# Performance work log

Hardware: AMD Instinct MI355X
Metric: run time of the kernel (lower is better)

Reference implementation:

```python
import jax, jax.numpy as jnp
import numpy as np

NCODEBOOKS, K, SUBVEC = 32, 16, 128
IN_F, OUT_F = 4096, 2048
BATCH, SEQ = 2, 1024


def setup_inputs() -> dict:
    key = jax.random.key(0)
    k1, k2, k3, k4, k5 = jax.random.split(key, 5)
    return {
        "x": jax.random.normal(k1, (BATCH, SEQ, IN_F), dtype=jnp.float32),
        "centroids": jax.random.normal(k2, (NCODEBOOKS, K, SUBVEC), dtype=jnp.float32),
        "weight": jax.random.normal(k3, (NCODEBOOKS, SUBVEC, OUT_F), dtype=jnp.float32),
        "inverse_temperature_logit": jax.random.normal(k4, (1,), dtype=jnp.float32),
        "bias": jax.random.normal(k5, (OUT_F,), dtype=jnp.float32),
    }


def reference(x, centroids, weight, inverse_temperature_logit, bias):
    shape = x.shape[:-1]
    C, k, d = centroids.shape
    # [N, C, d] -> [C, N, d]
    xr = jnp.transpose(x.reshape(-1, C, d), (1, 0, 2))
    # Euclidean cdist per codebook: [C, N, k]
    x2 = jnp.sum(xr * xr, axis=-1)[:, :, None]
    c2 = jnp.sum(centroids * centroids, axis=-1)[:, None, :]
    xc = jnp.einsum('cnd,ckd->cnk', xr, centroids)
    dist = jnp.sqrt(jnp.maximum(x2 + c2 - 2.0 * xc, 0.0))
    inv_temp = jax.nn.softplus(inverse_temperature_logit) + 1.0  # [1]
    attention = jax.nn.softmax(-dist * inv_temp, axis=-1)  # [C, N, k]
    lut = jnp.einsum('ckd,cdo->cko', centroids, weight)  # [C, k, O]
    training_output = jnp.einsum('cnk,cko->no', attention, lut)  # [N, O]
    # one-hot argmin matmul == direct gather of lut rows
    idx = jnp.argmin(dist, axis=-1)  # [C, N]
    gathered = jnp.take_along_axis(lut, idx[:, :, None], axis=1)  # [C, N, O]
    inference_output = jnp.sum(gathered, axis=0)  # [N, O]
    # straight-through estimator
    output = training_output - jax.lax.stop_gradient(training_output - inference_output)
    output = output + bias
    return output.reshape(*shape, lut.shape[-1])
```

## Files before the change

### kernel.cpp

```cpp
#include <hip/hip_runtime.h>

#define NCB 32
#define KK 16
#define DD 128
#define IN_F 4096
#define OUT_F 2048
#define NTOK 2048

#define LUT_BLOCKS 256
#define TT 32
#define IDX_BLOCKS ((NTOK / TT) * NCB)

#define XS_STRIDE 148
#define CS_OFF (TT * XS_STRIDE)
#define SMEM_FLOATS (CS_OFF + KK * 164)

__global__ __launch_bounds__(256, 4) void fused_lut_idx(
    const float* __restrict__ centroids, const float* __restrict__ weight,
    const float* __restrict__ x, const float* __restrict__ bias,
    float* __restrict__ lut, unsigned char* __restrict__ idxb) {
    __shared__ float smem[SMEM_FLOATS];
    const int tid = threadIdx.x;

    if (blockIdx.x < LUT_BLOCKS) {
        const int c  = blockIdx.x >> 3;
        const int ot = blockIdx.x & 7;
        const int kq = __builtin_amdgcn_readfirstlane(tid >> 6);
        const int o  = ot * 256 + (tid & 63) * 4;
        const float* cb = centroids + ((size_t)c * KK + kq * 4) * DD;
        const float* wb = weight + (size_t)c * DD * OUT_F + o;
        float4 acc[4];
#pragma unroll
        for (int k = 0; k < 4; ++k) acc[k] = make_float4(0.f, 0.f, 0.f, 0.f);
#pragma unroll 2
        for (int d4 = 0; d4 < DD / 4; ++d4) {
            float4 w0 = *(const float4*)(wb + (size_t)(d4 * 4 + 0) * OUT_F);
            float4 w1 = *(const float4*)(wb + (size_t)(d4 * 4 + 1) * OUT_F);
            float4 w2 = *(const float4*)(wb + (size_t)(d4 * 4 + 2) * OUT_F);
            float4 w3 = *(const float4*)(wb + (size_t)(d4 * 4 + 3) * OUT_F);
#pragma unroll
            for (int k = 0; k < 4; ++k) {
                float4 cv = *(const float4*)(cb + k * DD + d4 * 4);
                acc[k].x += cv.x * w0.x + cv.y * w1.x + cv.z * w2.x + cv.w * w3.x;
                acc[k].y += cv.x * w0.y + cv.y * w1.y + cv.z * w2.y + cv.w * w3.y;
                acc[k].z += cv.x * w0.z + cv.y * w1.z + cv.z * w2.z + cv.w * w3.z;
                acc[k].w += cv.x * w0.w + cv.y * w1.w + cv.z * w2.w + cv.w * w3.w;
            }
        }
        if (c == 0) {
            float4 bv = *(const float4*)(bias + o);
#pragma unroll
            for (int k = 0; k < 4; ++k) {
                acc[k].x += bv.x; acc[k].y += bv.y;
                acc[k].z += bv.z; acc[k].w += bv.w;
            }
        }
#pragma unroll
        for (int k = 0; k < 4; ++k)
            *(float4*)(lut + ((size_t)c * KK + kq * 4 + k) * OUT_F + o) = acc[k];
    } else {
        const int bid = blockIdx.x - LUT_BLOCKS;
        const int c = bid & (NCB - 1);
        const int t0 = (bid >> 5) * TT;
        const int th_q = tid & 3;
        const int th_k = (tid >> 2) & 3;
        const int th_t = tid >> 4;
        float* xs = smem;
        float* cs = smem + CS_OFF;

        {
            const float* xg = x + (size_t)t0 * IN_F + c * DD;
#pragma unroll
            for (int i = 0; i < (TT * DD / 4) / 256; ++i) {
                int p = i * 256 + tid;
                int t = p >> 5, f4 = p & 31;
                int q = f4 >> 3, jj = f4 & 7;
                float4 v = *(const float4*)(xg + (size_t)t * IN_F + f4 * 4);
                *(float4*)(xs + t * XS_STRIDE + q * 36 + jj * 4) = v;
            }
        }
        for (int p = tid; p < KK * 32; p += 256) {
            int k = p >> 5, f4 = p & 31;
            int q = f4 >> 3, jj = f4 & 7;
            *(float4*)(cs + k * 164 + q * 40 + jj * 4) =
                *(const float4*)(centroids + ((size_t)c * KK + k) * DD + f4 * 4);
        }
        __syncthreads();

        float acc[2][4], sq[4];
#pragma unroll
        for (int r = 0; r < 2; ++r)
#pragma unroll
            for (int kk = 0; kk < 4; ++kk) acc[r][kk] = 0.f;
#pragma unroll
        for (int kk = 0; kk < 4; ++kk) sq[kk] = 0.f;

#pragma unroll
        for (int chunk = 0; chunk < 8; ++chunk) {
            float4 ca[4];
#pragma unroll
            for (int kk = 0; kk < 4; ++kk)
                ca[kk] = *(const float4*)(cs + (th_k * 4 + kk) * 164 + th_q * 40 + chunk * 4);
#pragma unroll
            for (int kk = 0; kk < 4; ++kk)
                sq[kk] += ca[kk].x * ca[kk].x + ca[kk].y * ca[kk].y
                        + ca[kk].z * ca[kk].z + ca[kk].w * ca[kk].w;
#pragma unroll
            for (int r = 0; r < 2; ++r) {
                float4 xr = *(const float4*)(xs + (th_t * 2 + r) * XS_STRIDE
                                             + th_q * 36 + chunk * 4);
#pragma unroll
                for (int kk = 0; kk < 4; ++kk)
                    acc[r][kk] += xr.x * ca[kk].x + xr.y * ca[kk].y
                                + xr.z * ca[kk].z + xr.w * ca[kk].w;
            }
        }
#pragma unroll
        for (int kk = 0; kk < 4; ++kk) {
            float a = sq[kk];
            a += __shfl_xor(a, 1);
            a += __shfl_xor(a, 2);
            sq[kk] = a;
        }
#pragma unroll
        for (int r = 0; r < 2; ++r)
#pragma unroll
            for (int kk = 0; kk < 4; ++kk) {
                float a = acc[r][kk];
                a += __shfl_xor(a, 1);
                a += __shfl_xor(a, 2);
                acc[r][kk] = a;
            }
#pragma unroll
        for (int r = 0; r < 2; ++r) {
            float best = sq[0] - 2.f * acc[r][0];
            int bi = th_k * 4;
#pragma unroll
            for (int kk = 1; kk < 4; ++kk) {
                float v = sq[kk] - 2.f * acc[r][kk];
                if (v < best) { best = v; bi = th_k * 4 + kk; }
            }
#pragma unroll
            for (int s = 4; s <= 8; s <<= 1) {
                float ov = __shfl_xor(best, s);
                int oi = __shfl_xor(bi, s);
                if (ov < best || (ov == best && oi < bi)) { best = ov; bi = oi; }
            }
            if ((tid & 15) == 0)
                idxb[(size_t)(t0 + th_t * 2 + r) * NCB + c] = (unsigned char)bi;
        }
    }
}

__global__ __launch_bounds__(256) void gather_kernel(const float* __restrict__ lut,
                                                     const unsigned char* __restrict__ idxb,
                                                     float* __restrict__ out) {
    const int o0 = blockIdx.x * 32;
    const int t0 = blockIdx.y * 64;
    const int og = threadIdx.x & 7;
    const int tl = threadIdx.x >> 3;
    const int o = o0 + og * 4;

    const int ta = t0 + tl;
    const int tb = ta + 32;
    const uint4 ivA0 = *(const uint4*)(idxb + (size_t)ta * NCB);
    const uint4 ivA1 = *(const uint4*)(idxb + (size_t)ta * NCB + 16);
    const uint4 ivB0 = *(const uint4*)(idxb + (size_t)tb * NCB);
    const uint4 ivB1 = *(const uint4*)(idxb + (size_t)tb * NCB + 16);
    unsigned int uA[8] = {ivA0.x, ivA0.y, ivA0.z, ivA0.w, ivA1.x, ivA1.y, ivA1.z, ivA1.w};
    unsigned int uB[8] = {ivB0.x, ivB0.y, ivB0.z, ivB0.w, ivB1.x, ivB1.y, ivB1.z, ivB1.w};

    float4 accA = make_float4(0.f, 0.f, 0.f, 0.f);
    float4 accB = make_float4(0.f, 0.f, 0.f, 0.f);
#pragma unroll
    for (int c4 = 0; c4 < 8; ++c4) {
        unsigned int uvA = uA[c4], uvB = uB[c4];
#pragma unroll
        for (int b = 0; b < 4; ++b) {
            int cc = c4 * 4 + b;
            int kA = (uvA >> (8 * b)) & 0xff;
            int kB = (uvB >> (8 * b)) & 0xff;
            const float4 vA = *(const float4*)(lut + (size_t)(cc * KK + kA) * OUT_F + o);
            const float4 vB = *(const float4*)(lut + (size_t)(cc * KK + kB) * OUT_F + o);
            accA.x += vA.x; accA.y += vA.y; accA.z += vA.z; accA.w += vA.w;
            accB.x += vB.x; accB.y += vB.y; accB.z += vB.z; accB.w += vB.w;
        }
    }
    *(float4*)(out + (size_t)ta * OUT_F + o) = accA;
    *(float4*)(out + (size_t)tb * OUT_F + o) = accB;
}

extern "C" void kernel_launch(void* const* d_in, const int* in_sizes, int n_in,
                              void* d_out, int out_size, void* d_ws, size_t ws_size,
                              hipStream_t stream) {
    const float* x         = (const float*)d_in[0];
    const float* centroids = (const float*)d_in[1];
    const float* weight    = (const float*)d_in[2];
    const float* bias      = (const float*)d_in[4];
    float* out = (float*)d_out;

    float* lut = (float*)d_ws;
    unsigned char* idxb = (unsigned char*)d_ws + (4u << 20);

    fused_lut_idx<<<LUT_BLOCKS + IDX_BLOCKS, 256, 0, stream>>>(
        centroids, weight, x, bias, lut, idxb);
    gather_kernel<<<dim3(OUT_F / 32, NTOK / 64), 256, 0, stream>>>(lut, idxb, out);
}
```

Baseline: 152.6 us.

## Stage weight tiles through shared memory with register prefetch in LUT blocks

In the LUT-building blocks, the four wavefronts each used to load the same weight rows straight from global memory. Those rows are now loaded once per block into shared memory in 16-row stages, with the next stage prefetched into registers while the current one is computed. This cuts redundant global and L2 traffic for the weight tensor by up to a factor of four. The cost is extra LDS reads and two barriers per stage, which could throttle the idx blocks that run in the same launch.

Result: slower. 219.9 us (+44.1%).

```diff
diff --git a/kernel.cpp b/kernel.cpp
--- a/kernel.cpp
+++ b/kernel.cpp
@@ -25,30 +25,63 @@
     if (blockIdx.x < LUT_BLOCKS) {
         const int c  = blockIdx.x >> 3;
         const int ot = blockIdx.x & 7;
+        const int o0 = ot * 256;
+        const int j  = tid & 63;
         const int kq = __builtin_amdgcn_readfirstlane(tid >> 6);
-        const int o  = ot * 256 + (tid & 63) * 4;
         const float* cb = centroids + ((size_t)c * KK + kq * 4) * DD;
-        const float* wb = weight + (size_t)c * DD * OUT_F + o;
+        const float* wg = weight + (size_t)c * DD * OUT_F + o0;
+        float* wt = smem;
+
+        const int srow = tid >> 6;
         float4 acc[4];
 #pragma unroll
         for (int k = 0; k < 4; ++k) acc[k] = make_float4(0.f, 0.f, 0.f, 0.f);
-#pragma unroll 2
-        for (int d4 = 0; d4 < DD / 4; ++d4) {
-            float4 w0 = *(const float4*)(wb + (size_t)(d4 * 4 + 0) * OUT_F);
-            float4 w1 = *(const float4*)(wb + (size_t)(d4 * 4 + 1) * OUT_F);
-            float4 w2 = *(const float4*)(wb + (size_t)(d4 * 4 + 2) * OUT_F);
-            float4 w3 = *(const float4*)(wb + (size_t)(d4 * 4 + 3) * OUT_F);
-#pragma unroll
-            for (int k = 0; k < 4; ++k) {
-                float4 cv = *(const float4*)(cb + k * DD + d4 * 4);
-                acc[k].x += cv.x * w0.x + cv.y * w1.x + cv.z * w2.x + cv.w * w3.x;
-                acc[k].y += cv.x * w0.y + cv.y * w1.y + cv.z * w2.y + cv.w * w3.y;
-                acc[k].z += cv.x * w0.z + cv.y * w1.z + cv.z * w2.z + cv.w * w3.z;
-                acc[k].w += cv.x * w0.w + cv.y * w1.w + cv.z * w2.w + cv.w * w3.w;
+
+        float4 rv[4];
+#pragma unroll
+        for (int i = 0; i < 4; ++i) {
+            int row = i * 4 + srow;
+            rv[i] = *(const float4*)(wg + (size_t)row * OUT_F + j * 4);
+        }
+#pragma unroll
+        for (int i = 0; i < 4; ++i)
+            *(float4*)(wt + (i * 4 + srow) * 256 + j * 4) = rv[i];
+        __syncthreads();
+
+#pragma unroll
+        for (int s = 0; s < 8; ++s) {
+            if (s < 7) {
+#pragma unroll
+                for (int i = 0; i < 4; ++i) {
+                    int row = (s + 1) * 16 + i * 4 + srow;
+                    rv[i] = *(const float4*)(wg + (size_t)row * OUT_F + j * 4);
+                }
+            }
+#pragma unroll
+            for (int d4 = 0; d4 < 4; ++d4) {
+                float4 w0 = *(const float4*)(wt + (d4 * 4 + 0) * 256 + j * 4);
+                float4 w1 = *(const float4*)(wt + (d4 * 4 + 1) * 256 + j * 4);
+                float4 w2 = *(const float4*)(wt + (d4 * 4 + 2) * 256 + j * 4);
+                float4 w3 = *(const float4*)(wt + (d4 * 4 + 3) * 256 + j * 4);
+#pragma unroll
+                for (int k = 0; k < 4; ++k) {
+                    float4 cv = *(const float4*)(cb + k * DD + s * 16 + d4 * 4);
+                    acc[k].x += cv.x * w0.x + cv.y * w1.x + cv.z * w2.x + cv.w * w3.x;
+                    acc[k].y += cv.x * w0.y + cv.y * w1.y + cv.z * w2.y + cv.w * w3.y;
+                    acc[k].z += cv.x * w0.z + cv.y * w1.z + cv.z * w2.z + cv.w * w3.z;
+                    acc[k].w += cv.x * w0.w + cv.y * w1.w + cv.z * w2.w + cv.w * w3.w;
+                }
+            }
+            if (s < 7) {
+                __syncthreads();
+#pragma unroll
+                for (int i = 0; i < 4; ++i)
+                    *(float4*)(wt + (i * 4 + srow) * 256 + j * 4) = rv[i];
+                __syncthreads();
             }
         }
         if (c == 0) {
-            float4 bv = *(const float4*)(bias + o);
+            float4 bv = *(const float4*)(bias + o0 + j * 4);
 #pragma unroll
             for (int k = 0; k < 4; ++k) {
                 acc[k].x += bv.x; acc[k].y += bv.y;
@@ -57,7 +90,7 @@
         }
 #pragma unroll
         for (int k = 0; k < 4; ++k)
-            *(float4*)(lut + ((size_t)c * KK + kq * 4 + k) * OUT_F + o) = acc[k];
+            *(float4*)(lut + ((size_t)c * KK + kq * 4 + k) * OUT_F + o0 + j * 4) = acc[k];
     } else {
         const int bid = blockIdx.x - LUT_BLOCKS;
         const int c = bid & (NCB - 1);
```
